# Optimization experiments

Measured on AMD Instinct MI355X. Metric: run time of the kernel, lower is better.

The kernel has to match this reference:

```python
import jax, jax.numpy as jnp
import numpy as np

OBS, ACT, NTRAIN, BATCH = 8, 4, 128, 8
DIN = OBS + ACT


def setup_inputs() -> dict:
    key = jax.random.key(0)
    ks = jax.random.split(key, 11)
    f32 = jnp.float32
    m_x = jax.random.normal(ks[0], (BATCH, OBS), dtype=f32)
    A = 0.1 * jax.random.normal(ks[1], (BATCH, OBS, OBS), dtype=f32)
    s_x = A @ jnp.swapaxes(A, -1, -2) + 0.01 * jnp.eye(OBS, dtype=f32)  # SPD obs covariance
    m_u = jax.random.normal(ks[2], (BATCH, ACT), dtype=f32)
    Au = 0.1 * jax.random.normal(ks[3], (BATCH, ACT, ACT), dtype=f32)
    s_u = Au @ jnp.swapaxes(Au, -1, -2) + 0.01 * jnp.eye(ACT, dtype=f32)
    c_xu = 0.05 * jax.random.normal(ks[4], (BATCH, OBS, ACT), dtype=f32)
    X_train = jax.random.normal(ks[5], (NTRAIN, DIN), dtype=f32)
    lengthscales = jax.random.uniform(ks[6], (OBS, DIN), dtype=f32, minval=0.5, maxval=2.0)
    variances = jax.random.uniform(ks[7], (OBS, 1), dtype=f32, minval=0.5, maxval=1.5)
    noises = jax.random.uniform(ks[8], (OBS,), dtype=f32, minval=0.01, maxval=0.1)
    R = jax.random.normal(ks[9], (OBS, NTRAIN, NTRAIN), dtype=f32) / np.float32(np.sqrt(NTRAIN))
    inv_K = R @ jnp.swapaxes(R, -1, -2) + 0.1 * jnp.eye(NTRAIN, dtype=f32)  # SPD like a true K^-1
    beta = 0.1 * jax.random.normal(ks[10], (OBS, NTRAIN), dtype=f32)
    return dict(m_x=m_x, s_x=s_x, m_u=m_u, s_u=s_u, c_xu=c_xu, X_train=X_train,
                lengthscales=lengthscales, variances=variances, noises=noises,
                inv_K=inv_K, beta=beta)


def _forward(m_x, s_x, m_u, s_u, c_xu, X_train, lengthscales, variances, noises, inv_K, beta):
    obs_dim, input_dim = lengthscales.shape
    n = X_train.shape[0]
    eyeD = jnp.eye(input_dim, dtype=m_x.dtype)
    # joint input distribution over [x, u]
    joint_mean = jnp.concatenate([m_x, m_u], axis=-1)                      # [B, D]
    s_ = s_x @ c_xu                                                        # [B, obs, act] (as in source)
    upper = jnp.concatenate([s_x, s_], axis=-1)                            # [B, obs, D]
    lower = jnp.concatenate([jnp.swapaxes(s_, -1, -2), s_u], axis=-1)      # [B, act, D]
    joint_var = jnp.concatenate([upper, lower], axis=-2)                   # [B, D, D]
    # --- predictive mean (moment matching) ---
    inp = X_train[None, :, :] - joint_mean[:, None, :]                     # [B, N, D]
    inv_ls = 1.0 / lengthscales                                            # [E, D]
    inv_N = inp[:, None, :, :] * inv_ls[None, :, None, :]                  # [B, E, N, D]
    B_mat = inv_ls[None, :, :, None] * joint_var[:, None, :, :] * inv_ls[None, :, None, :] + eyeD
    t = jnp.swapaxes(jnp.linalg.solve(B_mat, jnp.swapaxes(inv_N, -1, -2)), -1, -2)  # [B, E, N, D]
    scaled_exp = jnp.exp(-0.5 * jnp.sum(inv_N * t, axis=-1))               # [B, E, N]
    lb = scaled_exp * beta[None, :, :]                                     # [B, E, N]
    det_B = jnp.linalg.det(B_mat)                                          # [B, E]
    var_v = variances[:, 0]                                                # [E]
    c = var_v[None, :] / jnp.sqrt(det_B)                                   # [B, E]
    pred_mean = jnp.sum(lb, axis=-1) * c                                   # [B, E]
    # --- input-output cross covariance ---
    t_inv_L = t * inv_ls[None, :, None, :]                                 # [B, E, N, D]
    cross_cov = jnp.swapaxes(jnp.einsum('bend,ben->bed', t_inv_L, lb) * c[..., None], -1, -2)  # [B, D, E]
    # --- predictive covariance: vectorized over all (a, b) output pairs ---
    X_i = X_train[:, None, :]
    X_j = X_train[None, :, :]
    diff = X_i - X_j                                                       # [N, N, D]
    l2 = lengthscales ** 2
    inv_l2 = 1.0 / l2

    def pair(l2_a, inv_a, var_a, beta_a, l2_b, inv_b, var_b, beta_b):
        inv_sum = inv_a + inv_b                                            # [D]
        Lam = 1.0 / inv_sum
        z_bar = Lam * (X_i * inv_a + X_j * inv_b)                          # [N, N, D]
        z = z_bar[None, :, :, :] - joint_mean[:, None, None, :]            # [B, N, N, D]
        z_flat = z.reshape(z.shape[0], n * n, input_dim)
        R_ab = joint_var * inv_sum[None, None, :] + eyeD                   # joint_var @ diag(inv_sum) + I
        exp1 = -0.5 * jnp.sum(diff * diff * (1.0 / (l2_a + l2_b)), axis=-1)  # [N, N]
        M_ab = joint_var + jnp.diag(Lam)[None, :, :]                       # [B, D, D]
        solved = jnp.swapaxes(jnp.linalg.solve(M_ab, jnp.swapaxes(z_flat, -1, -2)), -1, -2)
        exp2 = (-0.5 * jnp.sum(z_flat * solved, axis=-1)).reshape(z.shape[0], n, n)
        c_ab = var_a * var_b / jnp.sqrt(jnp.linalg.det(R_ab))              # [B]
        Q = c_ab[:, None, None] * jnp.exp(exp1[None, :, :] + exp2)         # [B, N, N]
        main = jnp.einsum('i,bij,j->b', beta_a, Q, beta_b)                 # [B]
        return main, Q

    pair_b = jax.vmap(pair, in_axes=(None, None, None, None, 0, 0, 0, 0))
    pair_ab = jax.vmap(pair_b, in_axes=(0, 0, 0, 0, None, None, None, None))
    main, Q = pair_ab(l2, inv_l2, var_v, beta, l2, inv_l2, var_v, beta)    # [E, E, B], [E, E, B, N, N]
    pred_cov = jnp.moveaxis(main, -1, 0)                                   # [B, E, E]
    idx = jnp.arange(obs_dim)
    Q_diag = Q[idx, idx]                                                   # [E, B, N, N]
    trace_val = jnp.einsum('eij,ebji->eb', inv_K, Q_diag)                  # [E, B]
    diag_corr = var_v[:, None] - trace_val + noises[:, None]               # [E, B]
    pred_cov = pred_cov + diag_corr.T[:, :, None] * jnp.eye(obs_dim, dtype=m_x.dtype)
    pred_cov = pred_cov - pred_mean[:, :, None] * pred_mean[:, None, :]
    pred_cov = 0.5 * (pred_cov + jnp.swapaxes(pred_cov, -1, -2))
    # --- propagate state moments ---
    cov_xf = upper @ cross_cov                                             # [B, obs, obs]
    m_out = m_x + pred_mean
    s_out = s_x + pred_cov + cov_xf + jnp.swapaxes(cov_xf, -1, -2)
    s_out = 0.5 * (s_out + jnp.swapaxes(s_out, -1, -2)) + 1e-8 * jnp.eye(obs_dim, dtype=m_x.dtype)
    return m_out, s_out


def reference(m_x, s_x, m_u, s_u, c_xu, X_train, lengthscales, variances, noises, inv_K, beta):
    return _forward(m_x, s_x, m_u, s_u, c_xu, X_train, lengthscales, variances, noises, inv_K, beta)
```

## Files before the change

### kernel.cpp

```cpp
#include <hip/hip_runtime.h>
#include <math.h>

#define OBS 8
#define ACT 4
#define DIN 12
#define NTRAIN 128
#define BATCH 8
#define NPAIR 36
#define NBLK (BATCH*NPAIR)
#define THREADS 512
#define HSTRIDE 16

#define WS_PM  0
#define WS_CC  64
#define WS_MN  832
#define WS_TR  1344
#define WS_CNT 1536

__global__ void __launch_bounds__(THREADS, 4) k_all(
    const float* __restrict__ m_x, const float* __restrict__ s_x,
    const float* __restrict__ m_u, const float* __restrict__ s_u,
    const float* __restrict__ c_xu, const float* __restrict__ X,
    const float* __restrict__ ls, const float* __restrict__ vars,
    const float* __restrict__ noises, const float* __restrict__ beta,
    const float* __restrict__ invK, float* __restrict__ ws,
    float* __restrict__ out)
{
    int blk = blockIdx.x, tid = threadIdx.x;
    int lane = tid & 63, w = tid >> 6;
    int b = blk / NPAIR;
    int rem = blk % NPAIR;
    int a = 0;
    while (rem >= OBS - a) { rem -= OBS - a; a++; }
    int c = a + rem;
    bool diag = (a == c);

    __shared__ float jvs[144];
    __shared__ float Wl[144];
    __shared__ float Wg[144];
    __shared__ float mu[DIN];
    __shared__ float sc_wsum[DIN], sc_iA[DIN], sc_qc[DIN], sc_lam[DIN], sc_isum[DIN], sc_il[DIN];
    __shared__ float s_cab, s_cgp;
    __shared__ __align__(16) float h[NTRAIN][HSTRIDE];
    __shared__ __align__(16) float2 bw[NTRAIN];
    __shared__ float red[8][13];
    __shared__ float redg[2][16];
    __shared__ unsigned int s_last;

    int j0 = 2*lane;
    float xa[12], xb[12], xi[12];
    {
        const float4* xr = (const float4*)(X + j0*DIN);
        float4 t0 = xr[0], t1 = xr[1], t2 = xr[2], t3 = xr[3], t4 = xr[4], t5 = xr[5];
        xa[0]=t0.x; xa[1]=t0.y; xa[2]=t0.z; xa[3]=t0.w;
        xa[4]=t1.x; xa[5]=t1.y; xa[6]=t1.z; xa[7]=t1.w;
        xa[8]=t2.x; xa[9]=t2.y; xa[10]=t2.z; xa[11]=t2.w;
        xb[0]=t3.x; xb[1]=t3.y; xb[2]=t3.z; xb[3]=t3.w;
        xb[4]=t4.x; xb[5]=t4.y; xb[6]=t4.z; xb[7]=t4.w;
        xb[8]=t5.x; xb[9]=t5.y; xb[10]=t5.z; xb[11]=t5.w;
    }
    if (tid < 256) {
        int rowi = tid & 127;
        const float4* xr = (const float4*)(X + rowi*DIN);
        float4 t0 = xr[0], t1 = xr[1], t2 = xr[2];
        xi[0]=t0.x; xi[1]=t0.y; xi[2]=t0.z; xi[3]=t0.w;
        xi[4]=t1.x; xi[5]=t1.y; xi[6]=t1.z; xi[7]=t1.w;
        xi[8]=t2.x; xi[9]=t2.y; xi[10]=t2.z; xi[11]=t2.w;
    }

    if (tid < 144) {
        int r = tid / 12, cl = tid % 12;
        float v;
        if (r < OBS && cl < OBS) {
            v = s_x[(b*OBS+r)*OBS + cl];
        } else if (r < OBS) {
            v = 0.f;
            #pragma unroll
            for (int k = 0; k < OBS; k++)
                v += s_x[(b*OBS+r)*OBS+k] * c_xu[(b*OBS+k)*ACT + (cl-OBS)];
        } else if (cl < OBS) {
            v = 0.f;
            #pragma unroll
            for (int k = 0; k < OBS; k++)
                v += s_x[(b*OBS+cl)*OBS+k] * c_xu[(b*OBS+k)*ACT + (r-OBS)];
        } else {
            v = s_u[(b*ACT+r-OBS)*ACT + (cl-OBS)];
        }
        jvs[tid] = v;
    } else if (tid >= 160 && tid < 172) {
        int d = tid - 160;
        mu[d] = (d < OBS) ? m_x[b*OBS+d] : m_u[b*ACT+d-OBS];
    } else if (tid >= 192 && tid < 204) {
        int d = tid - 192;
        float la = ls[a*DIN+d]; la *= la;
        float lc = ls[c*DIN+d]; lc *= lc;
        float ia = 1.f/la, ic = 1.f/lc;
        float is = ia + ic;
        float L  = 1.f/is;
        sc_wsum[d] = 1.f/(la+lc);
        sc_iA[d] = L*ia;
        sc_qc[d] = L*ic;
        sc_lam[d] = L;
        sc_isum[d] = is;
    } else if (tid >= 224 && tid < 236) {
        int d = tid - 224;
        sc_il[d] = 1.f / ls[a*DIN+d];
    }
    __syncthreads();

    if (tid < 64 && lane < 28) {
        int grp = lane >> 4;
        int base = grp << 4;
        int r = lane - base;
        int rr = (r < 12) ? r : 0;
        float row[12];
        if (grp == 0) {
            #pragma unroll
            for (int j = 0; j < 12; j++) row[j] = jvs[rr*12+j];
            row[rr] += sc_lam[rr];
        } else {
            float ir = sc_il[r];
            #pragma unroll
            for (int j = 0; j < 12; j++) row[j] = ir * sc_il[j] * jvs[r*12+j];
            row[r] += 1.f;
        }
        float det = 1.f;
        #pragma unroll
        for (int k = 0; k < 12; k++) {
            float p = __shfl(row[k], base + k);
            float ip = 1.f / p;
            det *= p;
            float prow[12];
            #pragma unroll
            for (int j = 0; j < 12; j++) prow[j] = __shfl(row[j], base + k) * ip;
            if (r == k) {
                #pragma unroll
                for (int j = 0; j < 12; j++) row[j] = prow[j];
                row[k] = ip;
            } else {
                float f = row[k];
                #pragma unroll
                for (int j = 0; j < 12; j++) if (j != k) row[j] -= f * prow[j];
                row[k] = -f * ip;
            }
        }
        if (r < 12) {
            float* W = grp ? Wg : Wl;
            #pragma unroll
            for (int j = 0; j < 12; j++) W[r*12+j] = row[j];
        }
        if (lane == 0) {
            float s = det;
            #pragma unroll
            for (int d = 0; d < 12; d++) s *= sc_isum[d];
            s_cab = vars[a]*vars[c] / sqrtf(s);
        }
        if (lane == 16) s_cgp = vars[a] / sqrtf(det);
    }
    __syncthreads();

    if (tid < NTRAIN) {
        int t = tid;
        float r[12], q[12]; float e1 = 0.f;
        #pragma unroll
        for (int d = 0; d < 12; d++) {
            r[d] = sc_iA[d]*xi[d] - mu[d];
            q[d] = sc_qc[d]*xi[d];
            e1 += sc_wsum[d]*xi[d]*xi[d];
        }
        float hrow[16];
        float alpha = 0.f, bq = 0.f;
        #pragma unroll
        for (int d = 0; d < 12; d++) {
            float u = 0.f, uq = 0.f;
            #pragma unroll
            for (int cl = 0; cl < 12; cl++) {
                float wv = Wl[d*12+cl];
                u  += wv*r[cl];
                uq += wv*q[cl];
            }
            alpha += r[d]*u;
            bq    += q[d]*uq;
            hrow[d] = sc_wsum[d]*xi[d] - u*sc_qc[d];
        }
        hrow[12] = -0.5f*(e1 + alpha);
        hrow[13] = beta[a*NTRAIN+t];
        hrow[14] = 0.f; hrow[15] = 0.f;
        float4* hp = (float4*)&h[t][0];
        hp[0] = make_float4(hrow[0],hrow[1],hrow[2],hrow[3]);
        hp[1] = make_float4(hrow[4],hrow[5],hrow[6],hrow[7]);
        hp[2] = make_float4(hrow[8],hrow[9],hrow[10],hrow[11]);
        hp[3] = make_float4(hrow[12],hrow[13],hrow[14],hrow[15]);
        bw[t] = make_float2(-0.5f*(e1 + bq), beta[c*NTRAIN+t]);
    } else if (diag && tid < 256) {
        int n = tid - 128;
        float iN[12], tv[12];
        #pragma unroll
        for (int d = 0; d < 12; d++) iN[d] = (xi[d] - mu[d]) * sc_il[d];
        float qq = 0.f;
        #pragma unroll
        for (int d = 0; d < 12; d++) {
            float u = 0.f;
            #pragma unroll
            for (int cl = 0; cl < 12; cl++) u += Wg[d*12+cl]*iN[cl];
            tv[d] = u; qq += iN[d]*u;
        }
        float lb = __expf(-0.5f*qq) * beta[a*NTRAIN+n];
        float vals[13];
        vals[0] = lb;
        #pragma unroll
        for (int d = 0; d < 12; d++) vals[1+d] = tv[d]*sc_il[d]*lb;
        #pragma unroll
        for (int v = 0; v < 13; v++)
            #pragma unroll
            for (int off = 32; off >= 1; off >>= 1) vals[v] += __shfl_xor(vals[v], off, 64);
        if (lane == 0) {
            #pragma unroll
            for (int v = 0; v < 13; v++) redg[w-2][v] = vals[v];
        }
    }
    __syncthreads();

    float4 bwv = ((const float4*)bw)[lane];
    float basej0 = bwv.x, wc0 = bwv.y, basej1 = bwv.z, wc1 = bwv.w;
    float am0 = 0.f, am1 = 0.f, at0 = 0.f, at1 = 0.f;
    const float2* Kb = (const float2*)(invK + a*NTRAIN*NTRAIN);
    #pragma unroll 4
    for (int k = 0; k < 16; k++) {
        int i = w + 8*k;
        const float4* hp = (const float4*)&h[i][0];
        float4 h0 = hp[0], h1 = hp[1], h2 = hp[2];
        float2 h3 = *(const float2*)&h[i][12];
        float sA0 = fmaf(h0.x,xa[0], fmaf(h0.y,xa[1], fmaf(h0.z,xa[2], h0.w*xa[3])));
        float sB0 = fmaf(h1.x,xa[4], fmaf(h1.y,xa[5], fmaf(h1.z,xa[6], h1.w*xa[7])));
        float sC0 = fmaf(h2.x,xa[8], fmaf(h2.y,xa[9], fmaf(h2.z,xa[10], h2.w*xa[11])));
        float sA1 = fmaf(h0.x,xb[0], fmaf(h0.y,xb[1], fmaf(h0.z,xb[2], h0.w*xb[3])));
        float sB1 = fmaf(h1.x,xb[4], fmaf(h1.y,xb[5], fmaf(h1.z,xb[6], h1.w*xb[7])));
        float sC1 = fmaf(h2.x,xb[8], fmaf(h2.y,xb[9], fmaf(h2.z,xb[10], h2.w*xb[11])));
        float e0  = __expf(sA0 + sB0 + sC0 + h3.x + basej0);
        float e1v = __expf(sA1 + sB1 + sC1 + h3.x + basej1);
        am0 = fmaf(h3.y, e0, am0);
        am1 = fmaf(h3.y, e1v, am1);
        if (diag) {
            float2 kv = Kb[i*64 + lane];
            at0 = fmaf(kv.x, e0, at0);
            at1 = fmaf(kv.y, e1v, at1);
        }
    }
    float accm = am0*wc0 + am1*wc1;
    float acct = at0 + at1;
    #pragma unroll
    for (int off = 32; off >= 1; off >>= 1) {
        accm += __shfl_xor(accm, off, 64);
        acct += __shfl_xor(acct, off, 64);
    }
    if (lane == 0) { red[w][0] = accm; red[w][1] = acct; }
    __syncthreads();
    if (tid == 0) {
        float m = 0.f, t = 0.f;
        #pragma unroll
        for (int v = 0; v < 8; v++) { m += red[v][0]; t += red[v][1]; }
        m *= s_cab; t *= s_cab;
        ws[WS_MN + b*64 + a*8 + c] = m;
        ws[WS_MN + b*64 + c*8 + a] = m;
        if (diag) ws[WS_TR + b*8 + a] = t;
    } else if (tid == 64 && diag) {
        float cn = s_cgp;
        ws[WS_PM + b*OBS + a] = cn*(redg[0][0]+redg[1][0]);
        #pragma unroll
        for (int d = 0; d < 12; d++)
            ws[WS_CC + (b*DIN+d)*OBS + a] = cn*(redg[0][1+d]+redg[1][1+d]);
    }
    __syncthreads();

    if (tid == 0) {
        __threadfence();
        unsigned int old = __hip_atomic_fetch_add(
            (unsigned int*)(ws + WS_CNT), 1u,
            __ATOMIC_ACQ_REL, __HIP_MEMORY_SCOPE_AGENT);
        s_last = (old == NBLK - 1) ? 1u : 0u;
    }
    __syncthreads();

    if (s_last) {
        __threadfence();
        float* epiSx = &h[0][0];
        float* epiPm = &h[64][0];
        epiSx[tid] = s_x[tid];
        if (tid < 64) epiPm[tid] = ws[WS_PM + tid];
        __syncthreads();
        int bb = w, t = lane;
        int r = t >> 3, cl = t & 7;
        const float* cc  = ws + WS_CC + bb*DIN*OBS;
        const float* mn  = ws + WS_MN + bb*64;
        const float* tr  = ws + WS_TR + bb*OBS;
        const float* sxs = epiSx + bb*64;
        const float* pm8 = epiPm + bb*8;
        float P = mn[r*8 + cl];
        if (r == cl) P += vars[r] - tr[r] + noises[r];
        P -= pm8[r]*pm8[cl];
        float cxf = 0.f, cxfT = 0.f;
        #pragma unroll
        for (int d = 0; d < 8; d++) {
            cxf  += sxs[r*8+d]  * cc[d*8+cl];
            cxfT += sxs[cl*8+d] * cc[d*8+r];
        }
        #pragma unroll
        for (int d = 0; d < 4; d++) {
            float jr = 0.f, jc = 0.f;
            #pragma unroll
            for (int k = 0; k < 8; k++) {
                float cx = c_xu[(bb*OBS+k)*ACT + d];
                jr += sxs[r*8+k]  * cx;
                jc += sxs[cl*8+k] * cx;
            }
            cxf  += jr * cc[(8+d)*8 + cl];
            cxfT += jc * cc[(8+d)*8 + r];
        }
        float S = sxs[r*8+cl] + P + cxf + cxfT;
        if (r == cl) S += 1e-8f;
        out[64 + bb*64 + t] = S;
        if (t < OBS) out[bb*OBS + t] = m_x[bb*OBS + t] + pm8[t];
    }
}

extern "C" void kernel_launch(void* const* d_in, const int* in_sizes, int n_in,
                              void* d_out, int out_size, void* d_ws, size_t ws_size,
                              hipStream_t stream) {
    const float* m_x    = (const float*)d_in[0];
    const float* s_x    = (const float*)d_in[1];
    const float* m_u    = (const float*)d_in[2];
    const float* s_u    = (const float*)d_in[3];
    const float* c_xu   = (const float*)d_in[4];
    const float* X      = (const float*)d_in[5];
    const float* ls     = (const float*)d_in[6];
    const float* vars   = (const float*)d_in[7];
    const float* noises = (const float*)d_in[8];
    const float* invK   = (const float*)d_in[9];
    const float* beta   = (const float*)d_in[10];
    float* out = (float*)d_out;
    float* ws  = (float*)d_ws;

    hipMemsetAsync((char*)d_ws + WS_CNT*sizeof(float), 0, 4, stream);
    k_all<<<NBLK, THREADS, 0, stream>>>(m_x, s_x, m_u, s_u, c_xu, X, ls, vars,
                                        noises, beta, invK, ws, out);
}
```

Measured before the change: 106.6 us.

## Split last-block atomic epilogue into a separate final kernel launch

Measured after the change: 92.91 us. 12.8% less time.

```diff
diff --git a/kernel.cpp b/kernel.cpp
--- a/kernel.cpp
+++ b/kernel.cpp
@@ -15,16 +15,14 @@
 #define WS_CC  64
 #define WS_MN  832
 #define WS_TR  1344
-#define WS_CNT 1536
-
-__global__ void __launch_bounds__(THREADS, 4) k_all(
+
+__global__ void __launch_bounds__(THREADS) k_fused(
     const float* __restrict__ m_x, const float* __restrict__ s_x,
     const float* __restrict__ m_u, const float* __restrict__ s_u,
     const float* __restrict__ c_xu, const float* __restrict__ X,
     const float* __restrict__ ls, const float* __restrict__ vars,
-    const float* __restrict__ noises, const float* __restrict__ beta,
-    const float* __restrict__ invK, float* __restrict__ ws,
-    float* __restrict__ out)
+    const float* __restrict__ beta, const float* __restrict__ invK,
+    float* __restrict__ ws)
 {
     int blk = blockIdx.x, tid = threadIdx.x;
     int lane = tid & 63, w = tid >> 6;
@@ -45,7 +43,6 @@
     __shared__ __align__(16) float2 bw[NTRAIN];
     __shared__ float red[8][13];
     __shared__ float redg[2][16];
-    __shared__ unsigned int s_last;
 
     int j0 = 2*lane;
     float xa[12], xb[12], xi[12];
@@ -271,57 +268,50 @@
         for (int d = 0; d < 12; d++)
             ws[WS_CC + (b*DIN+d)*OBS + a] = cn*(redg[0][1+d]+redg[1][1+d]);
     }
-    __syncthreads();
-
-    if (tid == 0) {
-        __threadfence();
-        unsigned int old = __hip_atomic_fetch_add(
-            (unsigned int*)(ws + WS_CNT), 1u,
-            __ATOMIC_ACQ_REL, __HIP_MEMORY_SCOPE_AGENT);
-        s_last = (old == NBLK - 1) ? 1u : 0u;
-    }
-    __syncthreads();
-
-    if (s_last) {
-        __threadfence();
-        float* epiSx = &h[0][0];
-        float* epiPm = &h[64][0];
-        epiSx[tid] = s_x[tid];
-        if (tid < 64) epiPm[tid] = ws[WS_PM + tid];
-        __syncthreads();
-        int bb = w, t = lane;
-        int r = t >> 3, cl = t & 7;
-        const float* cc  = ws + WS_CC + bb*DIN*OBS;
-        const float* mn  = ws + WS_MN + bb*64;
-        const float* tr  = ws + WS_TR + bb*OBS;
-        const float* sxs = epiSx + bb*64;
-        const float* pm8 = epiPm + bb*8;
-        float P = mn[r*8 + cl];
-        if (r == cl) P += vars[r] - tr[r] + noises[r];
-        P -= pm8[r]*pm8[cl];
-        float cxf = 0.f, cxfT = 0.f;
-        #pragma unroll
-        for (int d = 0; d < 8; d++) {
-            cxf  += sxs[r*8+d]  * cc[d*8+cl];
-            cxfT += sxs[cl*8+d] * cc[d*8+r];
-        }
-        #pragma unroll
-        for (int d = 0; d < 4; d++) {
-            float jr = 0.f, jc = 0.f;
-            #pragma unroll
-            for (int k = 0; k < 8; k++) {
-                float cx = c_xu[(bb*OBS+k)*ACT + d];
-                jr += sxs[r*8+k]  * cx;
-                jc += sxs[cl*8+k] * cx;
-            }
-            cxf  += jr * cc[(8+d)*8 + cl];
-            cxfT += jc * cc[(8+d)*8 + r];
-        }
-        float S = sxs[r*8+cl] + P + cxf + cxfT;
-        if (r == cl) S += 1e-8f;
-        out[64 + bb*64 + t] = S;
-        if (t < OBS) out[bb*OBS + t] = m_x[bb*OBS + t] + pm8[t];
-    }
+}
+
+__global__ void k_final(const float* __restrict__ m_x, const float* __restrict__ s_x,
+                        const float* __restrict__ c_xu, const float* __restrict__ vars,
+                        const float* __restrict__ noises, const float* __restrict__ ws,
+                        float* __restrict__ out) {
+    int b = blockIdx.x, t = threadIdx.x;
+    __shared__ float pm[OBS];
+    __shared__ float sxs[64];
+    const float* cc = ws + WS_CC + b*DIN*OBS;
+    const float* mn = ws + WS_MN + b*64;
+    const float* tr = ws + WS_TR + b*OBS;
+    sxs[t] = s_x[b*64 + t];
+    if (t < OBS) {
+        float p = ws[WS_PM + b*OBS + t];
+        pm[t] = p;
+        out[b*OBS + t] = m_x[b*OBS + t] + p;
+    }
+    __syncthreads();
+    int r = t >> 3, cl = t & 7;
+    float P = mn[r*8 + cl];
+    if (r == cl) P += vars[r] - tr[r] + noises[r];
+    P -= pm[r]*pm[cl];
+    float cxf = 0.f, cxfT = 0.f;
+    #pragma unroll
+    for (int d = 0; d < 8; d++) {
+        cxf  += sxs[r*8+d]  * cc[d*8+cl];
+        cxfT += sxs[cl*8+d] * cc[d*8+r];
+    }
+    #pragma unroll
+    for (int d = 0; d < 4; d++) {
+        float jr = 0.f, jc = 0.f;
+        #pragma unroll
+        for (int k = 0; k < 8; k++) {
+            float cx = c_xu[(b*OBS+k)*ACT + d];
+            jr += sxs[r*8+k]  * cx;
+            jc += sxs[cl*8+k] * cx;
+        }
+        cxf  += jr * cc[(8+d)*8 + cl];
+        cxfT += jc * cc[(8+d)*8 + r];
+    }
+    float S = sxs[r*8+cl] + P + cxf + cxfT;
+    if (r == cl) S += 1e-8f;
+    out[64 + b*64 + t] = S;
 }
 
 extern "C" void kernel_launch(void* const* d_in, const int* in_sizes, int n_in,
@@ -341,7 +331,7 @@
     float* out = (float*)d_out;
     float* ws  = (float*)d_ws;
 
-    hipMemsetAsync((char*)d_ws + WS_CNT*sizeof(float), 0, 4, stream);
-    k_all<<<NBLK, THREADS, 0, stream>>>(m_x, s_x, m_u, s_u, c_xu, X, ls, vars,
-                                        noises, beta, invK, ws, out);
+    k_fused<<<NBLK, THREADS, 0, stream>>>(m_x, s_x, m_u, s_u, c_xu, X, ls, vars,
+                                          beta, invK, ws);
+    k_final<<<BATCH, 64, 0, stream>>>(m_x, s_x, c_xu, vars, noises, ws, out);
 }
```
